# Performance work log

Measured on AMD Instinct MI355X. Metric: run time of the kernel, lower is better.

## Reference

```python
import jax, jax.numpy as jnp
import numpy as np
import math

D_MODEL = 1024
N_HEADS = 16
D_HEAD = D_MODEL // N_HEADS
DECAY_MAX = 0.99  # buggy torch init: only the LAST head's decay rate survives the loop
LN_EPS = 1e-5


def setup_inputs() -> dict:
    key = jax.random.key(0)
    ks = jax.random.split(key, 12)
    B, S = 2, 2048
    x = jax.random.normal(ks[0], (B, S, D_MODEL), dtype=jnp.float32)
    def w(k):
        return jax.random.normal(k, (D_MODEL, D_MODEL), dtype=jnp.float32) * 0.02
    return {
        "x": x,
        "Wq": w(ks[1]), "bq": jnp.zeros((D_MODEL,), jnp.float32),
        "Wk": w(ks[2]), "bk": jnp.zeros((D_MODEL,), jnp.float32),
        "Wv": w(ks[3]), "bv": jnp.zeros((D_MODEL,), jnp.float32),
        "Wg": w(ks[4]), "bg": jnp.zeros((D_MODEL,), jnp.float32),
        "Wo": w(ks[5]), "bo": jnp.zeros((D_MODEL,), jnp.float32),
        "gamma": jnp.ones((D_MODEL,), jnp.float32),
        "beta": jnp.zeros((D_MODEL,), jnp.float32),
    }


def _decay_mask(S):
    # faithful to torch buffer: decay_matrix[i,j] = DECAY_MAX**(i-j) for j<=i else 0
    i = jnp.arange(S, dtype=jnp.float32)[:, None]
    j = jnp.arange(S, dtype=jnp.float32)[None, :]
    diff = i - j
    return jnp.where(diff >= 0, jnp.power(jnp.float32(DECAY_MAX), diff), 0.0)  # [S,S]


def reference(x, Wq, bq, Wk, bk, Wv, bv, Wg, bg, Wo, bo, gamma, beta):
    B, S, D = x.shape
    H, DH = N_HEADS, D_HEAD
    # projections -> [B,H,S,DH]
    Q = (x @ Wq + bq).reshape(B, S, H, DH).transpose(0, 2, 1, 3)
    K = (x @ Wk + bk).reshape(B, S, H, DH).transpose(0, 2, 1, 3)
    V = (x @ Wv + bv).reshape(B, S, H, DH).transpose(0, 2, 1, 3)
    scores = jnp.einsum('bhsd,bhtd->bhst', Q, K) / math.sqrt(DH)  # [B,H,S,S]
    mask = _decay_mask(S)  # [S,S], broadcast over B,H (head-independent per torch bug)
    retained = jnp.einsum('bhst,bhtd->bhsd', scores * mask, V)
    retained = retained.transpose(0, 2, 1, 3).reshape(B, S, D)
    # LayerNorm over last dim
    mu = jnp.mean(retained, axis=-1, keepdims=True)
    var = jnp.var(retained, axis=-1, keepdims=True)
    normed = (retained - mu) * jax.lax.rsqrt(var + LN_EPS) * gamma + beta
    G = jax.nn.sigmoid(x @ Wg + bg)
    return (normed * G) @ Wo + bo  # dropout = identity (eval)
```

## Files before the change

kernel.cpp:

```cpp
#include <hip/hip_runtime.h>

typedef __attribute__((ext_vector_type(4))) float f32x4;
typedef __attribute__((ext_vector_type(8))) short bf16x8;
typedef unsigned short USHORT;

static __device__ __forceinline__ float bf2f(USHORT u) {
    return __uint_as_float(((unsigned)u) << 16);
}
static __device__ __forceinline__ USHORT f2bf(float f) {
    unsigned u = __float_as_uint(f);
    unsigned r = u + 0x7FFF + ((u >> 16) & 1);
    return (USHORT)(r >> 16);
}

#define GLDS16(gp, lp) __builtin_amdgcn_global_load_lds(                      \
    (const __attribute__((address_space(1))) unsigned int*)(gp),              \
    (__attribute__((address_space(3))) unsigned int*)(lp), 16, 0, 0)

#define FULL_BARRIER() asm volatile("s_waitcnt vmcnt(0) lgkmcnt(0)\ns_barrier" ::: "memory")

#define D64 0.52559648f
#define L2D (-0.014499569695115089f)

struct PrepArgs { const float* src[5]; USHORT* dst[5]; const float* x; USHORT* xb; };

__global__ __launch_bounds__(256) void k_prep(PrepArgs pa) {
    const int z = blockIdx.z;
    const int tid = threadIdx.x;
    __shared__ USHORT t[64][65];
    if (z < 5) {
        const float* __restrict__ W  = pa.src[z];
        USHORT* __restrict__      WT = pa.dst[z];
        const int k0 = blockIdx.y * 64, n0 = blockIdx.x * 64;
#pragma unroll
        for (int s = 0; s < 4; s++) {
            int slot = tid + s * 256;
            int row = slot >> 4, c4 = (slot & 15) * 4;
            float4 vv = *(const float4*)&W[(size_t)(k0 + row) * 1024 + n0 + c4];
            t[row][c4 + 0] = f2bf(vv.x);
            t[row][c4 + 1] = f2bf(vv.y);
            t[row][c4 + 2] = f2bf(vv.z);
            t[row][c4 + 3] = f2bf(vv.w);
        }
        __syncthreads();
#pragma unroll
        for (int s = 0; s < 2; s++) {
            int slot = tid + s * 256;
            int n = slot >> 3, c8 = (slot & 7) * 8;
            USHORT tmp[8];
#pragma unroll
            for (int u = 0; u < 8; u++) tmp[u] = t[c8 + u][n];
            *(int4*)&WT[(size_t)(n0 + n) * 1024 + k0 + c8] = *(int4*)tmp;
        }
    } else {
        const int bi = blockIdx.y * 16 + blockIdx.x;
        const float* xs = pa.x + (size_t)bi * 16384;
        USHORT* xd = pa.xb + (size_t)bi * 16384;
#pragma unroll
        for (int u = 0; u < 16; u++) {
            int idx = u * 1024 + tid * 4;
            float4 v = *(const float4*)&xs[idx];
            *(ushort4*)&xd[idx] = make_ushort4(f2bf(v.x), f2bf(v.y), f2bf(v.z), f2bf(v.w));
        }
    }
}

struct GArgs {
    const USHORT* A;
    const USHORT* G;
    const float*  gamma;
    const float*  beta;
    const float*  stats;
    int           ln;
    const USHORT* W[4];
    const float*  bias[4];
    void*         dst[4];
    USHORT*       dstv;
    float         scale[4];
    int           mode[4];
};

__global__ __launch_bounds__(256, 2) void k_gemm(GArgs ga) {
    const int z = blockIdx.z;
    const USHORT* __restrict__ BT = ga.W[z];
    __shared__ USHORT As[2][128 * 32];
    __shared__ USHORT Bs[2][128 * 32];
    const int tid = threadIdx.x;
    const int m0 = blockIdx.y * 128, n0 = blockIdx.x * 128;
    const int w = tid >> 6, l = tid & 63, lr = l & 15, q = l >> 4;
    const int wr = w >> 1, wc = w & 1;
    const int srow = tid >> 2, sco = (tid & 3) * 8;
    f32x4 acc[4][4] = {};
    float mu0 = 0.f, iv0 = 0.f, mu1 = 0.f, iv1 = 0.f;
    if (ga.ln) {
        float2 s0 = *(const float2*)&ga.stats[(m0 + srow) * 2];
        mu0 = s0.x * (1.0f / 1024.0f);
        iv0 = rsqrtf(fmaxf(s0.y * (1.0f / 1024.0f) - mu0 * mu0, 0.0f) + 1e-5f);
        float2 s1 = *(const float2*)&ga.stats[(m0 + srow + 64) * 2];
        mu1 = s1.x * (1.0f / 1024.0f);
        iv1 = rsqrtf(fmaxf(s1.y * (1.0f / 1024.0f) - mu1 * mu1, 0.0f) + 1e-5f);
    }
#define STAGE_A(kt_, buf_)                                                       \
    do {                                                                         \
        const int kk0 = (kt_) * 32;                                              \
        if (ga.ln) {                                                             \
            float4 g0 = *(const float4*)&ga.gamma[kk0 + sco];                    \
            float4 g1 = *(const float4*)&ga.gamma[kk0 + sco + 4];                \
            float4 b0 = *(const float4*)&ga.beta[kk0 + sco];                     \
            float4 b1 = *(const float4*)&ga.beta[kk0 + sco + 4];                 \
            float gmv[8] = {g0.x,g0.y,g0.z,g0.w,g1.x,g1.y,g1.z,g1.w};            \
            float btv[8] = {b0.x,b0.y,b0.z,b0.w,b1.x,b1.y,b1.z,b1.w};            \
            _Pragma("unroll")                                                    \
            for (int hrow = 0; hrow < 2; hrow++) {                               \
                float mu = hrow ? mu1 : mu0, iv = hrow ? iv1 : iv0;              \
                size_t off = (size_t)(m0 + srow + hrow * 64) * 1024 + kk0 + sco; \
                USHORT r8[8], g8[8], a8[8];                                      \
                *(int4*)r8 = *(const int4*)&ga.A[off];                           \
                *(int4*)g8 = *(const int4*)&ga.G[off];                           \
                _Pragma("unroll")                                                \
                for (int u = 0; u < 8; u++)                                      \
                    a8[u] = f2bf(((bf2f(r8[u]) - mu) * iv * gmv[u] + btv[u])     \
                                 * bf2f(g8[u]));                                 \
                *(int4*)&As[buf_][(srow + hrow * 64) * 32 + sco] = *(int4*)a8;   \
            }                                                                    \
        } else {                                                                 \
            GLDS16(&ga.A[(size_t)(m0 + srow) * 1024 + kk0 + sco],                \
                   &As[buf_][srow * 32 + sco]);                                  \
            GLDS16(&ga.A[(size_t)(m0 + srow + 64) * 1024 + kk0 + sco],           \
                   &As[buf_][(srow + 64) * 32 + sco]);                           \
        }                                                                        \
        GLDS16(&BT[(size_t)(n0 + srow) * 1024 + kk0 + sco],                      \
               &Bs[buf_][srow * 32 + sco]);                                      \
        GLDS16(&BT[(size_t)(n0 + srow + 64) * 1024 + kk0 + sco],                 \
               &Bs[buf_][(srow + 64) * 32 + sco]);                               \
    } while (0)
    STAGE_A(0, 0);
    for (int kt = 0; kt < 32; kt++) {
        const int cur = kt & 1;
        FULL_BARRIER();
        if (kt + 1 < 32) STAGE_A(kt + 1, 1 - cur);
        bf16x8 af[4], bfr[4];
#pragma unroll
        for (int mi = 0; mi < 4; mi++)
            af[mi] = *(const bf16x8*)&As[cur][(wr * 64 + mi * 16 + lr) * 32 + q * 8];
#pragma unroll
        for (int ni = 0; ni < 4; ni++)
            bfr[ni] = *(const bf16x8*)&Bs[cur][(wc * 64 + ni * 16 + lr) * 32 + q * 8];
#pragma unroll
        for (int mi = 0; mi < 4; mi++)
#pragma unroll
            for (int ni = 0; ni < 4; ni++)
                acc[mi][ni] = __builtin_amdgcn_mfma_f32_16x16x32_bf16(
                    af[mi], bfr[ni], acc[mi][ni], 0, 0, 0);
    }
#undef STAGE_A
    const float scale = ga.scale[z];
    const int mode = ga.mode[z];
    const float* __restrict__ bias = ga.bias[z];
#pragma unroll
    for (int ni = 0; ni < 4; ni++) {
        int col = n0 + wc * 64 + ni * 16 + lr;
        float bv = bias[col];
#pragma unroll
        for (int mi = 0; mi < 4; mi++) {
            int r0 = m0 + wr * 64 + mi * 16 + q * 4;
            float vr[4];
#pragma unroll
            for (int r = 0; r < 4; r++) {
                float v = acc[mi][ni][r] + bv;
                if (mode == 1) v = 1.0f / (1.0f + __expf(-v));
                vr[r] = v * scale;
            }
            if (mode == 4) {
                float d0 = exp2f(L2D * (float)(r0 & 63));
                vr[0] *= d0;
                vr[1] *= d0 * 0.99f;
                vr[2] *= d0 * 0.9801f;
                vr[3] *= d0 * 0.970299f;
            }
            if (mode == 3) {
                float* df = (float*)ga.dst[z];
#pragma unroll
                for (int r = 0; r < 4; r++)
                    df[(size_t)(r0 + r) * 1024 + col] = vr[r];
            } else if (mode == 2) {
                int b = r0 >> 11, s = r0 & 2047;
                int h = col >> 6, d = col & 63;
                const float NP1 = 1.0101010101010102f;
                float c0 = exp2f(-L2D * (float)(s & 63));
                float c1 = c0 * NP1, c2 = c1 * NP1, c3 = c2 * NP1;
                *(ushort4*)&ga.dstv[(size_t)(((b * 16 + h) * 64) + d) * 2048 + s] =
                    make_ushort4(f2bf(vr[0] * c0), f2bf(vr[1] * c1),
                                 f2bf(vr[2] * c2), f2bf(vr[3] * c3));
            } else {
                USHORT* db = (USHORT*)ga.dst[z];
#pragma unroll
                for (int r = 0; r < 4; r++)
                    db[(size_t)(r0 + r) * 1024 + col] = f2bf(vr[r]);
            }
        }
    }
}

__global__ __launch_bounds__(256) void k_attn_u(const USHORT* __restrict__ K,
                                                const USHORT* __restrict__ VT,
                                                float* __restrict__ U) {
    const int bh = blockIdx.x, c = blockIdx.y;
    const int b = bh >> 4, h = bh & 15;
    const int tid = threadIdx.x, w = tid >> 6, l = tid & 63, lr = l & 15, q = l >> 4;
    __shared__ USHORT KT[64 * 72];
    __shared__ USHORT Vs[64 * 72];
#pragma unroll
    for (int s = 0; s < 2; s++) {
        int slot = tid + s * 256;
        int row = slot >> 3, co = (slot & 7) * 8;
        USHORT kv[8];
        *(int4*)kv = *(const int4*)&K[(size_t)(b * 2048 + c * 64 + row) * 1024 + h * 64 + co];
#pragma unroll
        for (int u = 0; u < 8; u++) KT[(co + u) * 72 + row] = kv[u];
        *(int4*)&Vs[row * 72 + co] =
            *(const int4*)&VT[(size_t)(bh * 64 + row) * 2048 + c * 64 + co];
    }
    __syncthreads();
    f32x4 acc[4] = {};
    bf16x8 av[2];
#pragma unroll
    for (int kk = 0; kk < 2; kk++)
        av[kk] = *(const bf16x8*)&Vs[(w * 16 + lr) * 72 + kk * 32 + q * 8];
#pragma unroll
    for (int dkt = 0; dkt < 4; dkt++)
#pragma unroll
        for (int kk = 0; kk < 2; kk++) {
            bf16x8 bk = *(const bf16x8*)&KT[(dkt * 16 + lr) * 72 + kk * 32 + q * 8];
            acc[dkt] = __builtin_amdgcn_mfma_f32_16x16x32_bf16(av[kk], bk, acc[dkt], 0, 0, 0);
        }
    float* slot = U + (size_t)(bh * 32 + c) * 4096;
#pragma unroll
    for (int dkt = 0; dkt < 4; dkt++)
#pragma unroll
        for (int r = 0; r < 4; r++)
            slot[(w * 16 + q * 4 + r) * 64 + dkt * 16 + lr] = acc[dkt][r] * D64;
}

__global__ __launch_bounds__(256, 2) void k_apply(const USHORT* __restrict__ Q,
                                                  const USHORT* __restrict__ K,
                                                  const USHORT* __restrict__ VT,
                                                  const float* __restrict__ U,
                                                  USHORT* __restrict__ R,
                                                  float* __restrict__ stats) {
    const int bh = blockIdx.x, c = blockIdx.y;
    const int b = bh >> 4, h = bh & 15;
    const int i0 = c * 64;
    const int tid = threadIdx.x, w = tid >> 6, l = tid & 63, lr = l & 15, q = l >> 4;
    __shared__ USHORT Qs[64 * 72];
    __shared__ USHORT Ks[64 * 72];
    __shared__ USHORT Vs[64 * 72];
    __shared__ USHORT Ps[4][16 * 72];
    __shared__ unsigned Spk[4096];
#pragma unroll
    for (int s = 0; s < 2; s++) {
        int slot = tid + s * 256;
        int row = slot >> 3, c8 = (slot & 7) * 8;
        *(int4*)&Qs[row * 72 + c8] =
            *(const int4*)&Q[(size_t)(b * 2048 + i0 + row) * 1024 + h * 64 + c8];
        *(int4*)&Ks[row * 72 + c8] =
            *(const int4*)&K[(size_t)(b * 2048 + i0 + row) * 1024 + h * 64 + c8];
        *(int4*)&Vs[row * 72 + c8] =
            *(const int4*)&VT[(size_t)(bh * 64 + row) * 2048 + i0 + c8];
    }
    if (c > 0) {
        float sa[16] = {};
        const float* Ub = U + (size_t)bh * 32 * 4096 + tid * 16;
        for (int cp = 0; cp < c; cp++) {
            const float* p = Ub + (size_t)cp * 4096;
#pragma unroll
            for (int u4 = 0; u4 < 4; u4++) {
                float4 uv = *(const float4*)(p + u4 * 4);
                sa[u4 * 4 + 0] = sa[u4 * 4 + 0] * D64 + uv.x;
                sa[u4 * 4 + 1] = sa[u4 * 4 + 1] * D64 + uv.y;
                sa[u4 * 4 + 2] = sa[u4 * 4 + 2] * D64 + uv.z;
                sa[u4 * 4 + 3] = sa[u4 * 4 + 3] * D64 + uv.w;
            }
        }
#pragma unroll
        for (int u = 0; u < 16; u++) {
            USHORT hi = f2bf(sa[u]);
            float  lo = sa[u] - bf2f(hi);
            Spk[tid * 16 + u] = (unsigned)hi | ((unsigned)f2bf(lo) << 16);
        }
    }
    __syncthreads();
    bf16x8 bqf[2];
#pragma unroll
    for (int kk = 0; kk < 2; kk++)
        bqf[kk] = *(const bf16x8*)&Qs[(w * 16 + lr) * 72 + kk * 32 + q * 8];
    f32x4 accr[4] = {};
    if (c > 0) {
#pragma unroll
        for (int dt = 0; dt < 4; dt++)
#pragma unroll
            for (int kk = 0; kk < 2; kk++) {
                const unsigned* sp = &Spk[(dt * 16 + lr) * 64 + kk * 32 + q * 8];
                uint4 pa = *(const uint4*)sp;
                uint4 pb = *(const uint4*)(sp + 4);
                unsigned pk[8] = { pa.x, pa.y, pa.z, pa.w, pb.x, pb.y, pb.z, pb.w };
                bf16x8 hi, lo;
#pragma unroll
                for (int u = 0; u < 8; u++) {
                    hi[u] = (short)(pk[u] & 0xffffu);
                    lo[u] = (short)(pk[u] >> 16);
                }
                accr[dt] = __builtin_amdgcn_mfma_f32_16x16x32_bf16(hi, bqf[kk], accr[dt], 0, 0, 0);
                accr[dt] = __builtin_amdgcn_mfma_f32_16x16x32_bf16(lo, bqf[kk], accr[dt], 0, 0, 0);
            }
    }
    {
        f32x4 accp[4] = {};
#pragma unroll
        for (int kk = 0; kk < 2; kk++)
#pragma unroll
            for (int jt = 0; jt < 4; jt++) {
                bf16x8 akf = *(const bf16x8*)&Ks[(jt * 16 + lr) * 72 + kk * 32 + q * 8];
                accp[jt] = __builtin_amdgcn_mfma_f32_16x16x32_bf16(akf, bqf[kk], accp[jt], 0, 0, 0);
            }
        const int ii = w * 16 + lr;
#pragma unroll
        for (int jt = 0; jt < 4; jt++) {
            const int jj = jt * 16 + q * 4;
            float v0 = (jj + 0 <= ii) ? accp[jt][0] : 0.0f;
            float v1 = (jj + 1 <= ii) ? accp[jt][1] : 0.0f;
            float v2 = (jj + 2 <= ii) ? accp[jt][2] : 0.0f;
            float v3 = (jj + 3 <= ii) ? accp[jt][3] : 0.0f;
            unsigned w0 = __builtin_amdgcn_perm(
                __float_as_uint(v1), __float_as_uint(v0), 0x07060302u);
            unsigned w1 = __builtin_amdgcn_perm(
                __float_as_uint(v3), __float_as_uint(v2), 0x07060302u);
            *(uint2*)&Ps[w][lr * 72 + jt * 16 + q * 4] = make_uint2(w0, w1);
        }
        asm volatile("s_waitcnt lgkmcnt(0)" ::: "memory");
#pragma unroll
        for (int kk = 0; kk < 2; kk++) {
            bf16x8 bpf = *(const bf16x8*)&Ps[w][lr * 72 + kk * 32 + q * 8];
#pragma unroll
            for (int dt = 0; dt < 4; dt++) {
                bf16x8 avf = *(const bf16x8*)&Vs[(dt * 16 + lr) * 72 + kk * 32 + q * 8];
                accr[dt] = __builtin_amdgcn_mfma_f32_16x16x32_bf16(avf, bpf, accr[dt], 0, 0, 0);
            }
        }
    }
    {
        float s1 = 0.f, s2 = 0.f;
#pragma unroll
        for (int dt = 0; dt < 4; dt++)
#pragma unroll
            for (int r = 0; r < 4; r++) {
                float v = accr[dt][r];
                s1 += v; s2 += v * v;
            }
        s1 += __shfl_down(s1, 32); s2 += __shfl_down(s2, 32);
        s1 += __shfl_down(s1, 16); s2 += __shfl_down(s2, 16);
        if (q == 0) {
            int row = b * 2048 + i0 + w * 16 + lr;
            atomicAdd(&stats[row * 2 + 0], s1);
            atomicAdd(&stats[row * 2 + 1], s2);
        }
    }
    {
        const int i = i0 + w * 16 + lr;
#pragma unroll
        for (int dt = 0; dt < 4; dt++) {
            f32x4 a = accr[dt];
            *(ushort4*)&R[(size_t)(b * 2048 + i) * 1024 + h * 64 + dt * 16 + q * 4] =
                make_ushort4(f2bf(a[0]), f2bf(a[1]), f2bf(a[2]), f2bf(a[3]));
        }
    }
}

extern "C" void kernel_launch(void* const* d_in, const int* in_sizes, int n_in,
                              void* d_out, int out_size, void* d_ws, size_t ws_size,
                              hipStream_t stream) {
    const float* x     = (const float*)d_in[0];
    const float* Wq    = (const float*)d_in[1];
    const float* bq    = (const float*)d_in[2];
    const float* Wk    = (const float*)d_in[3];
    const float* bk    = (const float*)d_in[4];
    const float* Wv    = (const float*)d_in[5];
    const float* bv    = (const float*)d_in[6];
    const float* Wg    = (const float*)d_in[7];
    const float* bg    = (const float*)d_in[8];
    const float* Wo    = (const float*)d_in[9];
    const float* bo    = (const float*)d_in[10];
    const float* gamma = (const float*)d_in[11];
    const float* beta  = (const float*)d_in[12];

    char* ws = (char*)d_ws;
    const size_t MB = 1 << 20;
    USHORT* WqT = (USHORT*)(ws + 0 * MB);
    USHORT* WkT = (USHORT*)(ws + 2 * MB);
    USHORT* WvT = (USHORT*)(ws + 4 * MB);
    USHORT* WgT = (USHORT*)(ws + 6 * MB);
    USHORT* WoT = (USHORT*)(ws + 8 * MB);
    USHORT* Qb  = (USHORT*)(ws + 10 * MB);
    USHORT* Kb  = (USHORT*)(ws + 18 * MB);
    USHORT* VTb = (USHORT*)(ws + 26 * MB);
    USHORT* Gb  = (USHORT*)(ws + 34 * MB);
    float*  Sts = (float*) (ws + 42 * MB);
    USHORT* Xb  = (USHORT*)d_out;
    float*  Ust = (float*)d_out;

    {
        PrepArgs pa;
        pa.src[0] = Wq; pa.src[1] = Wk; pa.src[2] = Wv; pa.src[3] = Wg; pa.src[4] = Wo;
        pa.dst[0] = WqT; pa.dst[1] = WkT; pa.dst[2] = WvT; pa.dst[3] = WgT; pa.dst[4] = WoT;
        pa.x = x; pa.xb = Xb;
        k_prep<<<dim3(16, 16, 6), 256, 0, stream>>>(pa);
    }
    hipMemsetAsync((void*)Sts, 0, 4096 * 2 * sizeof(float), stream);
    {
        GArgs ga;
        ga.A = Xb; ga.G = nullptr; ga.gamma = gamma; ga.beta = beta;
        ga.stats = Sts; ga.ln = 0;
        ga.W[0] = WqT; ga.W[1] = WkT; ga.W[2] = WvT; ga.W[3] = WgT;
        ga.bias[0] = bq; ga.bias[1] = bk; ga.bias[2] = bv; ga.bias[3] = bg;
        ga.dst[0] = Qb; ga.dst[1] = Kb; ga.dst[2] = nullptr; ga.dst[3] = Gb;
        ga.dstv = VTb;
        ga.scale[0] = 0.125f; ga.scale[1] = 1.0f; ga.scale[2] = 1.0f; ga.scale[3] = 1.0f;
        ga.mode[0] = 4; ga.mode[1] = 0; ga.mode[2] = 2; ga.mode[3] = 1;
        k_gemm<<<dim3(8, 32, 4), 256, 0, stream>>>(ga);
    }
    k_attn_u<<<dim3(32, 32), 256, 0, stream>>>(Kb, VTb, Ust);
    k_apply<<<dim3(32, 32), 256, 0, stream>>>(Qb, Kb, VTb, Ust, Kb, Sts);
    {
        GArgs go;
        go.A = Kb;
        go.G = Gb; go.gamma = gamma; go.beta = beta; go.stats = Sts; go.ln = 1;
        for (int i = 0; i < 4; i++) {
            go.W[i] = WoT; go.bias[i] = bo; go.dst[i] = d_out;
            go.scale[i] = 1.0f; go.mode[i] = 3;
        }
        go.dstv = nullptr;
        k_gemm<<<dim3(8, 32, 1), 256, 0, stream>>>(go);
    }
}
```

Measured before the change: 252.6 us.

## Split LayerNorm-gate into separate kernel, stream GEMM A-tiles via LDS DMA

Moves the LayerNorm and sigmoid-gate application out of the output GEMM's A-staging path into a new standalone k_ln_gate kernel that writes a bf16 normalized-gated tensor. Both GEMMs can then use direct global-to-LDS loads for A. Per-head row statistics are written to per-head slots instead of atomics, which also removes the stats memset. The Q decay scaling moves from the projection epilogue into k_apply's Q staging. The cost is an extra launch plus a write and reread of a 4096x1024 bf16 tensor, in exchange for a simpler, fully pipelined GEMM main loop and no atomic contention.

Measured after the change: 217.4 us. 1.16x faster.

```diff
diff --git a/kernel.cpp b/kernel.cpp
--- a/kernel.cpp
+++ b/kernel.cpp
@@ -67,11 +67,6 @@
 
 struct GArgs {
     const USHORT* A;
-    const USHORT* G;
-    const float*  gamma;
-    const float*  beta;
-    const float*  stats;
-    int           ln;
     const USHORT* W[4];
     const float*  bias[4];
     void*         dst[4];
@@ -82,6 +77,7 @@
 
 __global__ __launch_bounds__(256, 2) void k_gemm(GArgs ga) {
     const int z = blockIdx.z;
+    const USHORT* __restrict__ A  = ga.A;
     const USHORT* __restrict__ BT = ga.W[z];
     __shared__ USHORT As[2][128 * 32];
     __shared__ USHORT Bs[2][128 * 32];
@@ -91,54 +87,21 @@
     const int wr = w >> 1, wc = w & 1;
     const int srow = tid >> 2, sco = (tid & 3) * 8;
     f32x4 acc[4][4] = {};
-    float mu0 = 0.f, iv0 = 0.f, mu1 = 0.f, iv1 = 0.f;
-    if (ga.ln) {
-        float2 s0 = *(const float2*)&ga.stats[(m0 + srow) * 2];
-        mu0 = s0.x * (1.0f / 1024.0f);
-        iv0 = rsqrtf(fmaxf(s0.y * (1.0f / 1024.0f) - mu0 * mu0, 0.0f) + 1e-5f);
-        float2 s1 = *(const float2*)&ga.stats[(m0 + srow + 64) * 2];
-        mu1 = s1.x * (1.0f / 1024.0f);
-        iv1 = rsqrtf(fmaxf(s1.y * (1.0f / 1024.0f) - mu1 * mu1, 0.0f) + 1e-5f);
-    }
-#define STAGE_A(kt_, buf_)                                                       \
-    do {                                                                         \
-        const int kk0 = (kt_) * 32;                                              \
-        if (ga.ln) {                                                             \
-            float4 g0 = *(const float4*)&ga.gamma[kk0 + sco];                    \
-            float4 g1 = *(const float4*)&ga.gamma[kk0 + sco + 4];                \
-            float4 b0 = *(const float4*)&ga.beta[kk0 + sco];                     \
-            float4 b1 = *(const float4*)&ga.beta[kk0 + sco + 4];                 \
-            float gmv[8] = {g0.x,g0.y,g0.z,g0.w,g1.x,g1.y,g1.z,g1.w};            \
-            float btv[8] = {b0.x,b0.y,b0.z,b0.w,b1.x,b1.y,b1.z,b1.w};            \
-            _Pragma("unroll")                                                    \
-            for (int hrow = 0; hrow < 2; hrow++) {                               \
-                float mu = hrow ? mu1 : mu0, iv = hrow ? iv1 : iv0;              \
-                size_t off = (size_t)(m0 + srow + hrow * 64) * 1024 + kk0 + sco; \
-                USHORT r8[8], g8[8], a8[8];                                      \
-                *(int4*)r8 = *(const int4*)&ga.A[off];                           \
-                *(int4*)g8 = *(const int4*)&ga.G[off];                           \
-                _Pragma("unroll")                                                \
-                for (int u = 0; u < 8; u++)                                      \
-                    a8[u] = f2bf(((bf2f(r8[u]) - mu) * iv * gmv[u] + btv[u])     \
-                                 * bf2f(g8[u]));                                 \
-                *(int4*)&As[buf_][(srow + hrow * 64) * 32 + sco] = *(int4*)a8;   \
-            }                                                                    \
-        } else {                                                                 \
-            GLDS16(&ga.A[(size_t)(m0 + srow) * 1024 + kk0 + sco],                \
-                   &As[buf_][srow * 32 + sco]);                                  \
-            GLDS16(&ga.A[(size_t)(m0 + srow + 64) * 1024 + kk0 + sco],           \
-                   &As[buf_][(srow + 64) * 32 + sco]);                           \
-        }                                                                        \
-        GLDS16(&BT[(size_t)(n0 + srow) * 1024 + kk0 + sco],                      \
-               &Bs[buf_][srow * 32 + sco]);                                      \
-        GLDS16(&BT[(size_t)(n0 + srow + 64) * 1024 + kk0 + sco],                 \
-               &Bs[buf_][(srow + 64) * 32 + sco]);                               \
-    } while (0)
-    STAGE_A(0, 0);
+    GLDS16(&A [(size_t)(m0 + srow)      * 1024 + sco], &As[0][srow * 32 + sco]);
+    GLDS16(&A [(size_t)(m0 + srow + 64) * 1024 + sco], &As[0][(srow + 64) * 32 + sco]);
+    GLDS16(&BT[(size_t)(n0 + srow)      * 1024 + sco], &Bs[0][srow * 32 + sco]);
+    GLDS16(&BT[(size_t)(n0 + srow + 64) * 1024 + sco], &Bs[0][(srow + 64) * 32 + sco]);
     for (int kt = 0; kt < 32; kt++) {
         const int cur = kt & 1;
         FULL_BARRIER();
-        if (kt + 1 < 32) STAGE_A(kt + 1, 1 - cur);
+        if (kt + 1 < 32) {
+            const int k1 = (kt + 1) * 32;
+            const int nxt = 1 - cur;
+            GLDS16(&A [(size_t)(m0 + srow)      * 1024 + k1 + sco], &As[nxt][srow * 32 + sco]);
+            GLDS16(&A [(size_t)(m0 + srow + 64) * 1024 + k1 + sco], &As[nxt][(srow + 64) * 32 + sco]);
+            GLDS16(&BT[(size_t)(n0 + srow)      * 1024 + k1 + sco], &Bs[nxt][srow * 32 + sco]);
+            GLDS16(&BT[(size_t)(n0 + srow + 64) * 1024 + k1 + sco], &Bs[nxt][(srow + 64) * 32 + sco]);
+        }
         bf16x8 af[4], bfr[4];
 #pragma unroll
         for (int mi = 0; mi < 4; mi++)
@@ -153,7 +116,6 @@
                 acc[mi][ni] = __builtin_amdgcn_mfma_f32_16x16x32_bf16(
                     af[mi], bfr[ni], acc[mi][ni], 0, 0, 0);
     }
-#undef STAGE_A
     const float scale = ga.scale[z];
     const int mode = ga.mode[z];
     const float* __restrict__ bias = ga.bias[z];
@@ -170,13 +132,6 @@
                 float v = acc[mi][ni][r] + bv;
                 if (mode == 1) v = 1.0f / (1.0f + __expf(-v));
                 vr[r] = v * scale;
-            }
-            if (mode == 4) {
-                float d0 = exp2f(L2D * (float)(r0 & 63));
-                vr[0] *= d0;
-                vr[1] *= d0 * 0.99f;
-                vr[2] *= d0 * 0.9801f;
-                vr[3] *= d0 * 0.970299f;
             }
             if (mode == 3) {
                 float* df = (float*)ga.dst[z];
@@ -261,8 +216,12 @@
     for (int s = 0; s < 2; s++) {
         int slot = tid + s * 256;
         int row = slot >> 3, c8 = (slot & 7) * 8;
-        *(int4*)&Qs[row * 72 + c8] =
-            *(const int4*)&Q[(size_t)(b * 2048 + i0 + row) * 1024 + h * 64 + c8];
+        USHORT q8[8];
+        *(int4*)q8 = *(const int4*)&Q[(size_t)(b * 2048 + i0 + row) * 1024 + h * 64 + c8];
+        const float fr = exp2f(L2D * (float)row);
+#pragma unroll
+        for (int u = 0; u < 8; u++) q8[u] = f2bf(bf2f(q8[u]) * fr);
+        *(int4*)&Qs[row * 72 + c8] = *(int4*)q8;
         *(int4*)&Ks[row * 72 + c8] =
             *(const int4*)&K[(size_t)(b * 2048 + i0 + row) * 1024 + h * 64 + c8];
         *(int4*)&Vs[row * 72 + c8] =
@@ -361,8 +320,7 @@
         s1 += __shfl_down(s1, 16); s2 += __shfl_down(s2, 16);
         if (q == 0) {
             int row = b * 2048 + i0 + w * 16 + lr;
-            atomicAdd(&stats[row * 2 + 0], s1);
-            atomicAdd(&stats[row * 2 + 1], s2);
+            *(float2*)&stats[((size_t)row * 16 + h) * 2] = make_float2(s1, s2);
         }
     }
     {
@@ -374,6 +332,40 @@
                 make_ushort4(f2bf(a[0]), f2bf(a[1]), f2bf(a[2]), f2bf(a[3]));
         }
     }
+}
+
+__global__ __launch_bounds__(256) void k_ln_gate(const USHORT* __restrict__ R,
+                                                 const USHORT* __restrict__ G,
+                                                 const float* __restrict__ stats,
+                                                 const float* __restrict__ gamma,
+                                                 const float* __restrict__ beta,
+                                                 USHORT* __restrict__ NG) {
+    const int row = blockIdx.x, tid = threadIdx.x;
+    float s1 = 0.f, s2 = 0.f;
+    const float* sp = &stats[(size_t)row * 32];
+#pragma unroll
+    for (int hh = 0; hh < 8; hh++) {
+        float4 v = *(const float4*)(sp + hh * 4);
+        s1 += v.x + v.z; s2 += v.y + v.w;
+    }
+    const float mu  = s1 * (1.0f / 1024.0f);
+    const float var = s2 * (1.0f / 1024.0f) - mu * mu;
+    const float inv = rsqrtf(fmaxf(var, 0.0f) + 1e-5f);
+    ushort4 rv = *(const ushort4*)&R[(size_t)row * 1024 + tid * 4];
+    ushort4 g4 = *(const ushort4*)&G[(size_t)row * 1024 + tid * 4];
+    float4 gm = *(const float4*)&gamma[tid * 4];
+    float4 bt = *(const float4*)&beta[tid * 4];
+    float  vv[4]  = { bf2f(rv.x), bf2f(rv.y), bf2f(rv.z), bf2f(rv.w) };
+    USHORT gg[4]  = { g4.x, g4.y, g4.z, g4.w };
+    float  gmm[4] = { gm.x, gm.y, gm.z, gm.w };
+    float  btt[4] = { bt.x, bt.y, bt.z, bt.w };
+    USHORT o4[4];
+#pragma unroll
+    for (int u = 0; u < 4; u++) {
+        float nv = (vv[u] - mu) * inv * gmm[u] + btt[u];
+        o4[u] = f2bf(nv * bf2f(gg[u]));
+    }
+    *(ushort4*)&NG[(size_t)row * 1024 + tid * 4] = make_ushort4(o4[0], o4[1], o4[2], o4[3]);
 }
 
 extern "C" void kernel_launch(void* const* d_in, const int* in_sizes, int n_in,
@@ -405,6 +397,7 @@
     USHORT* VTb = (USHORT*)(ws + 26 * MB);
     USHORT* Gb  = (USHORT*)(ws + 34 * MB);
     float*  Sts = (float*) (ws + 42 * MB);
+    USHORT* NGb = Qb;
     USHORT* Xb  = (USHORT*)d_out;
     float*  Ust = (float*)d_out;
 
@@ -415,25 +408,23 @@
         pa.x = x; pa.xb = Xb;
         k_prep<<<dim3(16, 16, 6), 256, 0, stream>>>(pa);
     }
-    hipMemsetAsync((void*)Sts, 0, 4096 * 2 * sizeof(float), stream);
     {
         GArgs ga;
-        ga.A = Xb; ga.G = nullptr; ga.gamma = gamma; ga.beta = beta;
-        ga.stats = Sts; ga.ln = 0;
+        ga.A = Xb;
         ga.W[0] = WqT; ga.W[1] = WkT; ga.W[2] = WvT; ga.W[3] = WgT;
         ga.bias[0] = bq; ga.bias[1] = bk; ga.bias[2] = bv; ga.bias[3] = bg;
         ga.dst[0] = Qb; ga.dst[1] = Kb; ga.dst[2] = nullptr; ga.dst[3] = Gb;
         ga.dstv = VTb;
         ga.scale[0] = 0.125f; ga.scale[1] = 1.0f; ga.scale[2] = 1.0f; ga.scale[3] = 1.0f;
-        ga.mode[0] = 4; ga.mode[1] = 0; ga.mode[2] = 2; ga.mode[3] = 1;
+        ga.mode[0] = 0; ga.mode[1] = 0; ga.mode[2] = 2; ga.mode[3] = 1;
         k_gemm<<<dim3(8, 32, 4), 256, 0, stream>>>(ga);
     }
     k_attn_u<<<dim3(32, 32), 256, 0, stream>>>(Kb, VTb, Ust);
     k_apply<<<dim3(32, 32), 256, 0, stream>>>(Qb, Kb, VTb, Ust, Kb, Sts);
+    k_ln_gate<<<4096, 256, 0, stream>>>(Kb, Gb, Sts, gamma, beta, NGb);
     {
         GArgs go;
-        go.A = Kb;
-        go.G = Gb; go.gamma = gamma; go.beta = beta; go.stats = Sts; go.ln = 1;
+        go.A = NGb;
         for (int i = 0; i < 4; i++) {
             go.W[i] = WoT; go.bias[i] = bo; go.dst[i] = d_out;
             go.scale[i] = 1.0f; go.mode[i] = 3;
```
